# Kernel tuning notes

Measured on AMD Instinct MI355X. Metric: run time of the kernel, lower is better.

Reference implementation:

```python
import jax, jax.numpy as jnp
import numpy as np

B, T, D, DE, S, P = 16384, 2, 1024, 512, 4, 4  # batch, tasks, inp_dim, expt_dim, share, specific


def setup_inputs() -> dict:
    key = jax.random.key(0)
    ks = jax.random.split(key, 8)
    sc = 0.02
    return {
        "x0": jax.random.normal(ks[0], (B, D), jnp.float32),
        "x1": jax.random.normal(ks[1], (B, D), jnp.float32),
        "W_share": jax.random.normal(ks[2], (S, D, DE), jnp.float32) * sc,
        "b_share": jnp.zeros((S, DE), jnp.float32),
        "W_spcf": jax.random.normal(ks[3], (T, P, D, DE), jnp.float32) * sc,
        "b_spcf": jnp.zeros((T, P, DE), jnp.float32),
        "W_gate": jax.random.normal(ks[4], (T, D, S + P), jnp.float32) * sc,
        "b_gate": jnp.zeros((T, S + P), jnp.float32),
    }


def reference(x0, x1, W_share, b_share, W_spcf, b_spcf, W_gate, b_gate):
    # cat_x: [B, T, D]
    x = jnp.stack([x0, x1], axis=1)
    # per-task gate over all S+P experts: [B, T, S+P]
    gates = jax.nn.softmax(jnp.einsum("btd,tde->bte", x, W_gate) + b_gate, axis=-1)
    # shared experts applied to every task's input: [B, T, S, DE]
    share = jax.nn.relu(jnp.einsum("btd,sdf->btsf", x, W_share) + b_share[None, None])
    # task-specific experts applied to their own task input: [B, T, P, DE]
    spcf = jax.nn.relu(jnp.einsum("btd,tpdf->btpf", x, W_spcf) + b_spcf[None])
    experts = jnp.concatenate([share, spcf], axis=2)  # [B, T, S+P, DE]
    # softmax-gated mixture: [B, T, DE] (== list of per-task [B, DE] in the original)
    return jnp.einsum("bte,btef->btf", gates, experts)
```

## Files before the change

kernel.cpp:

```cpp
#include <hip/hip_runtime.h>
#include <stdint.h>

#define kB  16384
#define kD  1024
#define kDE 512

typedef __bf16 bf16x8 __attribute__((ext_vector_type(8)));
typedef float  f32x4  __attribute__((ext_vector_type(4)));

__device__ __forceinline__ unsigned short f2bf(float f) {
    union { float f; unsigned u; } v; v.f = f;
    unsigned r = v.u + 0x7FFFu + ((v.u >> 16) & 1u);
    return (unsigned short)(r >> 16);
}

__device__ __forceinline__ void async16(unsigned short* lds, const unsigned short* g) {
    __builtin_amdgcn_global_load_lds(
        (const __attribute__((address_space(1))) unsigned int*)g,
        (__attribute__((address_space(3))) unsigned int*)lds, 16, 0, 0);
}

__global__ __launch_bounds__(256) void prep_w(const float* __restrict__ Wsh,
                                              const float* __restrict__ Wsp,
                                              unsigned short* __restrict__ Wt) {
    __shared__ float tile[32][33];
    const int slot = blockIdx.z;
    const int k0 = blockIdx.x * 32;
    const int n0 = blockIdx.y * 32;
    const float* src = (slot < 4) ? (Wsh + (size_t)slot * kD * kDE)
                                  : (Wsp + (size_t)(slot - 4) * kD * kDE);
    const int tx = threadIdx.x, ty = threadIdx.y;
#pragma unroll
    for (int i = 0; i < 4; i++)
        tile[ty + i * 8][tx] = src[(size_t)(k0 + ty + i * 8) * kDE + n0 + tx];
    __syncthreads();
    unsigned short* dst = Wt + (size_t)slot * kDE * kD;
#pragma unroll
    for (int i = 0; i < 4; i++)
        dst[(size_t)(n0 + ty + i * 8) * kD + k0 + tx] = f2bf(tile[tx][ty + i * 8]);
}

__global__ __launch_bounds__(256) void prep_b(const float* __restrict__ bsh,
                                              const float* __restrict__ bsp,
                                              float* __restrict__ bc) {
    int i = blockIdx.x * 256 + threadIdx.x;
    int n = i & 511, e = (i >> 9) & 7, t = i >> 12;
    bc[i] = (e < 4) ? bsh[e * 512 + n] : bsp[(t * 4 + (e - 4)) * 512 + n];
}

__global__ __launch_bounds__(256) void conv_gate(
    const float* __restrict__ x0, const float* __restrict__ x1,
    const float* __restrict__ Wg, const float* __restrict__ bg,
    unsigned short* __restrict__ xb, float* __restrict__ g) {
    const int wid = threadIdx.x >> 6, lane = threadIdx.x & 63;
    const int r = blockIdx.x * 4 + wid;
    const int t = r >> 14, b = r & 16383;
    const float* xrow = (t ? x1 : x0) + (size_t)b * kD;
    unsigned short* xbrow = xb + (size_t)(t * kB + b) * kD;
    const float* Wgt = Wg + t * kD * 8;
    float p[8] = {0.f,0.f,0.f,0.f,0.f,0.f,0.f,0.f};
#pragma unroll
    for (int it = 0; it < 4; it++) {
        const int d0 = it * 256 + lane * 4;
        const float4 v = *(const float4*)(xrow + d0);
        ushort4 h;
        h.x = f2bf(v.x); h.y = f2bf(v.y); h.z = f2bf(v.z); h.w = f2bf(v.w);
        *(ushort4*)(xbrow + d0) = h;
        const float xv[4] = {v.x, v.y, v.z, v.w};
#pragma unroll
        for (int j = 0; j < 4; j++) {
            const float* wrow = Wgt + (size_t)(d0 + j) * 8;
#pragma unroll
            for (int e = 0; e < 8; e++) p[e] += xv[j] * wrow[e];
        }
    }
#pragma unroll
    for (int e = 0; e < 8; e++) {
        float v = p[e];
#pragma unroll
        for (int s = 1; s < 64; s <<= 1) v += __shfl_xor(v, s, 64);
        p[e] = v;
    }
    float lg[8];
#pragma unroll
    for (int e = 0; e < 8; e++) lg[e] = p[e] + bg[t * 8 + e];
    float mx = lg[0];
#pragma unroll
    for (int e = 1; e < 8; e++) mx = fmaxf(mx, lg[e]);
    float s = 0.f;
#pragma unroll
    for (int e = 0; e < 8; e++) { lg[e] = __expf(lg[e] - mx); s += lg[e]; }
    const float inv = 1.f / s;
    if (lane == 0) {
        float* gp = g + (size_t)(t * kB + b) * 8;
        float4 g0 = {lg[0]*inv, lg[1]*inv, lg[2]*inv, lg[3]*inv};
        float4 g1 = {lg[4]*inv, lg[5]*inv, lg[6]*inv, lg[7]*inv};
        *(float4*)gp = g0;
        *(float4*)(gp + 4) = g1;
    }
}

__global__ __launch_bounds__(512, 2) void moe_gemm(
    const unsigned short* __restrict__ xb, const unsigned short* __restrict__ Wt,
    const float* __restrict__ g, const float* __restrict__ bc,
    float* __restrict__ out) {
    __shared__ __align__(16) unsigned short As[2][128 * 64];
    __shared__ __align__(16) unsigned short Bs[2][8 * 64 * 64];

    const int bid = blockIdx.x;
    const int swz = (bid & 7) * 256 + (bid >> 3);
    const int ct = swz & 7;
    const int rt = (swz >> 3) & 127;
    const int t  = swz >> 10;
    const int n0 = ct * 64;

    const int tid = threadIdx.x, wid = tid >> 6, lane = tid & 63;
    const int wr = wid >> 2, wc = wid & 3;

    const int swzChunk = ((lane & 7) ^ ((lane >> 3) & 7)) * 8;
    const unsigned short* aSrc = xb + (size_t)t * kB * kD +
        (size_t)(rt * 128 + wid * 16 + (lane >> 3)) * kD + swzChunk;
    const int slot = (wid < 4) ? wid : (4 + t * 4 + (wid - 4));
    const unsigned short* bSrc = Wt + (size_t)slot * kDE * kD +
        (size_t)(n0 + (lane >> 3)) * kD + swzChunk;

    const int rAbase = (wr * 64 + (lane & 15)) * 64;
    const int bOff   = (wc * 16 + (lane & 15)) * 64;
    const int lx     = lane & 7;
    const int kg     = lane >> 4;

    f32x4 acc[8][4];
#pragma unroll
    for (int e = 0; e < 8; e++)
#pragma unroll
        for (int m = 0; m < 4; m++) acc[e][m] = (f32x4){0.f, 0.f, 0.f, 0.f};

#define STAGE(buf, kt)                                                        \
    {                                                                         \
        const int k0_ = (kt) * 64;                                            \
        _Pragma("unroll")                                                     \
        for (int i = 0; i < 2; i++)                                           \
            async16(&As[buf][wid * 1024 + i * 512], aSrc + k0_ + i * 8 * kD); \
        _Pragma("unroll")                                                     \
        for (int j = 0; j < 8; j++)                                           \
            async16(&Bs[buf][wid * 4096 + j * 512], bSrc + k0_ + j * 8 * kD); \
    }

#define COMPUTE(buf)                                                          \
    {                                                                         \
        _Pragma("unroll")                                                     \
        for (int ks = 0; ks < 2; ks++) {                                      \
            const int p8 = ((ks * 4 + kg) ^ lx) * 8;                          \
            bf16x8 af[4];                                                     \
            _Pragma("unroll")                                                 \
            for (int m = 0; m < 4; m++)                                       \
                af[m] = *(const bf16x8*)&As[buf][rAbase + m * 1024 + p8];     \
            _Pragma("unroll")                                                 \
            for (int e = 0; e < 8; e++) {                                     \
                bf16x8 bf = *(const bf16x8*)&Bs[buf][e * 4096 + bOff + p8];   \
                _Pragma("unroll")                                             \
                for (int m = 0; m < 4; m++)                                   \
                    acc[e][m] = __builtin_amdgcn_mfma_f32_16x16x32_bf16(      \
                        af[m], bf, acc[e][m], 0, 0, 0);                       \
            }                                                                 \
        }                                                                     \
    }

    STAGE(0, 0);
    for (int kt = 0; kt < 15; ++kt) {
        STAGE((kt + 1) & 1, kt + 1);
        asm volatile("s_waitcnt vmcnt(10)" ::: "memory");
        __builtin_amdgcn_s_barrier();
        COMPUTE(kt & 1);
        __builtin_amdgcn_s_barrier();
    }
    asm volatile("s_waitcnt vmcnt(0)" ::: "memory");
    __builtin_amdgcn_s_barrier();
    COMPUTE(1);

    const int col = n0 + wc * 16 + (lane & 15);
    float bv[8];
#pragma unroll
    for (int e = 0; e < 8; e++) bv[e] = bc[(t * 8 + e) * kDE + col];

#pragma unroll
    for (int m = 0; m < 4; m++) {
        const int r0 = rt * 128 + wr * 64 + m * 16 + kg * 4;
        f32x4 oq = (f32x4){0.f, 0.f, 0.f, 0.f};
#pragma unroll
        for (int q = 0; q < 4; q++) {
            const float* gp = g + ((size_t)t * kB + r0 + q) * 8;
            const float4 ga = *(const float4*)gp;
            const float4 gb = *(const float4*)(gp + 4);
            const float gv[8] = {ga.x, ga.y, ga.z, ga.w, gb.x, gb.y, gb.z, gb.w};
            float s = 0.f;
#pragma unroll
            for (int e = 0; e < 8; e++)
                s += gv[e] * fmaxf(acc[e][m][q] + bv[e], 0.f);
            oq[q] = s;
        }
#pragma unroll
        for (int q = 0; q < 4; q++)
            out[((size_t)(r0 + q) * 2 + t) * kDE + col] = oq[q];
    }
#undef STAGE
#undef COMPUTE
}

extern "C" void kernel_launch(void* const* d_in, const int* in_sizes, int n_in,
                              void* d_out, int out_size, void* d_ws, size_t ws_size,
                              hipStream_t stream) {
    const float* x0  = (const float*)d_in[0];
    const float* x1  = (const float*)d_in[1];
    const float* Wsh = (const float*)d_in[2];
    const float* bsh = (const float*)d_in[3];
    const float* Wsp = (const float*)d_in[4];
    const float* bsp = (const float*)d_in[5];
    const float* Wg  = (const float*)d_in[6];
    const float* bg  = (const float*)d_in[7];
    float* out = (float*)d_out;

    char* ws = (char*)d_ws;
    unsigned short* xb = (unsigned short*)ws;
    unsigned short* Wt = (unsigned short*)(ws + 67108864);
    float* g  = (float*)(ws + 67108864 + 12582912);
    float* bc = (float*)(ws + 67108864 + 12582912 + 1048576);

    prep_w<<<dim3(32, 16, 12), dim3(32, 8), 0, stream>>>(Wsh, Wsp, Wt);
    prep_b<<<dim3(32), dim3(256), 0, stream>>>(bsh, bsp, bc);
    conv_gate<<<dim3(8192), dim3(256), 0, stream>>>(x0, x1, Wg, bg, xb, g);
    moe_gemm<<<dim3(2048), dim3(512), 0, stream>>>(xb, Wt, g, bc, out);
}
```

Before: 415.7 us.

## Interleave async global-to-LDS loads with MFMA clusters in double-buffered GEMM loop

Restructures the K loop so the next tile's B loads are issued in pieces between four MFMA clusters instead of all at once before compute, with intermediate barriers and s_setprio raising priority during MFMA bursts. The loop is unrolled by two buffers, and the final iteration issues a dummy prefetch of tile 0 (wrapped index) rather than a separate tail compute. The aim is to hide global-load latency and smooth issue contention between memory and matrix instructions. It adds more barriers per step and a wasted extra load at the end.

Measured after the change: 450.4 us. +8.3%, slower.

```diff
diff --git a/kernel.cpp b/kernel.cpp
--- a/kernel.cpp
+++ b/kernel.cpp
@@ -135,48 +135,91 @@
 #pragma unroll
         for (int m = 0; m < 4; m++) acc[e][m] = (f32x4){0.f, 0.f, 0.f, 0.f};
 
-#define STAGE(buf, kt)                                                        \
-    {                                                                         \
-        const int k0_ = (kt) * 64;                                            \
-        _Pragma("unroll")                                                     \
-        for (int i = 0; i < 2; i++)                                           \
-            async16(&As[buf][wid * 1024 + i * 512], aSrc + k0_ + i * 8 * kD); \
-        _Pragma("unroll")                                                     \
-        for (int j = 0; j < 8; j++)                                           \
-            async16(&Bs[buf][wid * 4096 + j * 512], bSrc + k0_ + j * 8 * kD); \
-    }
-
-#define COMPUTE(buf)                                                          \
-    {                                                                         \
-        _Pragma("unroll")                                                     \
-        for (int ks = 0; ks < 2; ks++) {                                      \
-            const int p8 = ((ks * 4 + kg) ^ lx) * 8;                          \
-            bf16x8 af[4];                                                     \
-            _Pragma("unroll")                                                 \
-            for (int m = 0; m < 4; m++)                                       \
-                af[m] = *(const bf16x8*)&As[buf][rAbase + m * 1024 + p8];     \
-            _Pragma("unroll")                                                 \
-            for (int e = 0; e < 8; e++) {                                     \
-                bf16x8 bf = *(const bf16x8*)&Bs[buf][e * 4096 + bOff + p8];   \
-                _Pragma("unroll")                                             \
-                for (int m = 0; m < 4; m++)                                   \
-                    acc[e][m] = __builtin_amdgcn_mfma_f32_16x16x32_bf16(      \
-                        af[m], bf, acc[e][m], 0, 0, 0);                       \
-            }                                                                 \
-        }                                                                     \
-    }
-
-    STAGE(0, 0);
-    for (int kt = 0; kt < 15; ++kt) {
-        STAGE((kt + 1) & 1, kt + 1);
-        asm volatile("s_waitcnt vmcnt(10)" ::: "memory");
-        __builtin_amdgcn_s_barrier();
-        COMPUTE(kt & 1);
-        __builtin_amdgcn_s_barrier();
+    bf16x8 af[4];
+    bf16x8 bfr[4];
+
+#define STAGE_A(buf, ktn)                                                      \
+    _Pragma("unroll")                                                          \
+    for (int i = 0; i < 2; i++)                                                \
+        async16(&As[buf][wid * 1024 + i * 512], aSrc + (ktn) * 64 + i * 8 * kD);
+
+#define STAGE_B(buf, ktn, j0, jn)                                              \
+    _Pragma("unroll")                                                          \
+    for (int j = (j0); j < (j0) + (jn); j++)                                   \
+        async16(&Bs[buf][wid * 4096 + j * 512], bSrc + (ktn) * 64 + j * 8 * kD);
+
+#define READ_A(buf, ks)                                                        \
+    _Pragma("unroll")                                                          \
+    for (int m = 0; m < 4; m++)                                                \
+        af[m] = *(const bf16x8*)&As[buf][rAbase + m * 1024 +                   \
+                                         ((((ks) * 4 + kg) ^ lx) << 3)];
+
+#define READ_B(buf, ks, e0)                                                    \
+    _Pragma("unroll")                                                          \
+    for (int i = 0; i < 4; i++)                                                \
+        bfr[i] = *(const bf16x8*)&Bs[buf][((e0) + i) * 4096 + bOff +           \
+                                          ((((ks) * 4 + kg) ^ lx) << 3)];
+
+#define MFMA_CLUSTER(e0)                                                       \
+    asm volatile("s_waitcnt lgkmcnt(0)" ::: "memory");                         \
+    __builtin_amdgcn_sched_barrier(0);                                         \
+    __builtin_amdgcn_s_setprio(1);                                             \
+    _Pragma("unroll")                                                          \
+    for (int i = 0; i < 4; i++)                                                \
+        _Pragma("unroll")                                                      \
+        for (int m = 0; m < 4; m++)                                            \
+            acc[(e0) + i][m] = __builtin_amdgcn_mfma_f32_16x16x32_bf16(        \
+                af[m], bfr[i], acc[(e0) + i][m], 0, 0, 0);                     \
+    __builtin_amdgcn_s_setprio(0);
+
+#define STEP(cur, nxt, ktn)                                                    \
+    {                                                                          \
+                           \
+        STAGE_A(nxt, ktn);                                                     \
+        asm volatile("s_waitcnt vmcnt(2)" ::: "memory");                       \
+        __builtin_amdgcn_s_barrier();                                          \
+        __builtin_amdgcn_sched_barrier(0);                                     \
+        READ_A(cur, 0);                                                        \
+        READ_B(cur, 0, 0);                                                     \
+        MFMA_CLUSTER(0);                                                       \
+                                                     \
+        READ_B(cur, 0, 4);                                                     \
+        STAGE_B(nxt, ktn, 0, 3);                                               \
+        __builtin_amdgcn_s_barrier();                                          \
+        MFMA_CLUSTER(4);                                                       \
+                                                     \
+        READ_A(cur, 1);                                                        \
+        READ_B(cur, 1, 0);                                                     \
+        STAGE_B(nxt, ktn, 3, 3);                                               \
+        __builtin_amdgcn_s_barrier();                                          \
+        MFMA_CLUSTER(0);                                                       \
+                                                     \
+        READ_B(cur, 1, 4);                                                     \
+        STAGE_B(nxt, ktn, 6, 2);                                               \
+        __builtin_amdgcn_s_barrier();                                          \
+        MFMA_CLUSTER(4);                                                       \
+           \
+        __builtin_amdgcn_s_barrier();                                          \
+        __builtin_amdgcn_sched_barrier(0);                                     \
+    }
+
+    STAGE_A(0, 0);
+    STAGE_B(0, 0, 0, 8);
+
+    for (int kt2 = 0; kt2 < 8; ++kt2) {
+        const int ka = kt2 * 2 + 1;
+        const int kb = (kt2 * 2 + 2) & 15;
+        STEP(0, 1, ka)
+        STEP(1, 0, kb)
     }
     asm volatile("s_waitcnt vmcnt(0)" ::: "memory");
-    __builtin_amdgcn_s_barrier();
-    COMPUTE(1);
+
+#undef STAGE_A
+#undef STAGE_B
+#undef READ_A
+#undef READ_B
+#undef MFMA_CLUSTER
+#undef STEP
 
     const int col = n0 + wc * 16 + (lane & 15);
     float bv[8];
@@ -203,8 +246,6 @@
         for (int q = 0; q < 4; q++)
             out[((size_t)(r0 + q) * 2 + t) * kDE + col] = oq[q];
     }
-#undef STAGE
-#undef COMPUTE
 }
 
 extern "C" void kernel_launch(void* const* d_in, const int* in_sizes, int n_in,
```
